# Optimization experiments

Hardware: AMD Instinct MI355X
Metric: run time of the kernel (lower is better)

## Reference

```python
import jax, jax.numpy as jnp
import numpy as np

N, D, H, DFF, NH = 8192, 128, 256, 2048, 2
HD = D // NH
DEG = 32
E = N * DEG
LN_EPS = 1e-5


def setup_inputs() -> dict:
    key = jax.random.key(0)
    ks = jax.random.split(key, 20)
    s = 0.02
    return {
        "x": jax.random.normal(ks[0], (N, D), jnp.float32),
        "edge_index": jax.random.randint(ks[1], (2, E), 0, N, jnp.int64),
        "beta": jnp.ones((), jnp.float32),  # AGNNConv learnable beta, init 1
        "in_proj_w": jax.random.normal(ks[2], (3 * D, D), jnp.float32) * s,
        "in_proj_b": jnp.zeros((3 * D,), jnp.float32),
        "out_proj_w": jax.random.normal(ks[3], (D, D), jnp.float32) * s,
        "out_proj_b": jnp.zeros((D,), jnp.float32),
        "ln1_g": jnp.ones((D,), jnp.float32),
        "ln1_b": jnp.zeros((D,), jnp.float32),
        "ff1_w": jax.random.normal(ks[4], (DFF, D), jnp.float32) * s,
        "ff1_b": jnp.zeros((DFF,), jnp.float32),
        "ff2_w": jax.random.normal(ks[5], (D, DFF), jnp.float32) * s,
        "ff2_b": jnp.zeros((D,), jnp.float32),
        "ln2_g": jnp.ones((D,), jnp.float32),
        "ln2_b": jnp.zeros((D,), jnp.float32),
        "fc_w": jax.random.normal(ks[6], (H, D), jnp.float32) * s,
        "fc_b": jnp.zeros((H,), jnp.float32),
        "head_w": jax.random.normal(ks[7], (2, H), jnp.float32) * s,
        "head_b": jnp.zeros((2,), jnp.float32),
    }


def _layernorm(x, g, b):
    mu = jnp.mean(x, axis=-1, keepdims=True)
    var = jnp.mean((x - mu) ** 2, axis=-1, keepdims=True)
    return (x - mu) * jax.lax.rsqrt(var + LN_EPS) * g + b


def _agnn(x, edge_index, beta):
    # PyG AGNNConv: add self-loops, cosine-sim attention, segment softmax over targets
    n = x.shape[0]
    loop = jnp.arange(n, dtype=edge_index.dtype)
    src = jnp.concatenate([edge_index[0], loop])  # message source j
    dst = jnp.concatenate([edge_index[1], loop])  # aggregation target i
    xn = x / jnp.maximum(jnp.linalg.norm(x, axis=-1, keepdims=True), 1e-12)
    alpha = beta * jnp.sum(xn[dst] * xn[src], axis=-1)  # [E+N]
    m = jax.ops.segment_max(alpha, dst, num_segments=n)
    e = jnp.exp(alpha - m[dst])
    z = jax.ops.segment_sum(e, dst, num_segments=n)
    w = e / z[dst]
    return jax.ops.segment_sum(w[:, None] * x[src], dst, num_segments=n)


def reference(x, edge_index, beta, in_proj_w, in_proj_b, out_proj_w, out_proj_b,
              ln1_g, ln1_b, ff1_w, ff1_b, ff2_w, ff2_b, ln2_g, ln2_b,
              fc_w, fc_b, head_w, head_b):
    h = _agnn(x, edge_index, beta)  # [N, D]
    # transformer sees shape [N, 1, D] with batch_first=False -> seq over all N nodes
    qkv = h @ in_proj_w.T + in_proj_b  # [N, 3D]
    q, k, v = jnp.split(qkv, 3, axis=-1)
    q = q.reshape(N, NH, HD).transpose(1, 0, 2)  # [h, N, hd]
    k = k.reshape(N, NH, HD).transpose(1, 0, 2)
    v = v.reshape(N, NH, HD).transpose(1, 0, 2)
    scores = jnp.einsum('hnd,hmd->hnm', q, k) / jnp.sqrt(jnp.float32(HD))
    attn = jax.nn.softmax(scores, axis=-1)
    o = jnp.einsum('hnm,hmd->hnd', attn, v).transpose(1, 0, 2).reshape(N, D)
    o = o @ out_proj_w.T + out_proj_b
    h = _layernorm(h + o, ln1_g, ln1_b)  # post-LN (norm_first=False)
    ff = jax.nn.relu(h @ ff1_w.T + ff1_b) @ ff2_w.T + ff2_b
    h = _layernorm(h + ff, ln2_g, ln2_b)
    h = jax.nn.relu(h @ fc_w.T + fc_b)
    return h @ head_w.T + head_b  # [N, 2]
```

## Files before the change

kernel.cpp:

```cpp
#include <hip/hip_runtime.h>


typedef __attribute__((ext_vector_type(4))) float  f32x4;
typedef __attribute__((ext_vector_type(8))) __bf16 bf16x8;

#define DEV __device__ __forceinline__

DEV unsigned short f2bf_bits(float f) {
  union { float f; unsigned u; } v; v.f = f;
  unsigned r = v.u + 0x7FFFu + ((v.u >> 16) & 1u);
  return (unsigned short)(r >> 16);
}

DEV __bf16 f2bf(float f) {
  union { unsigned short s; __bf16 b; } o; o.s = f2bf_bits(f);
  return o.b;
}

DEV f32x4 mfma16(bf16x8 a, bf16x8 b, f32x4 c) {
  return __builtin_amdgcn_mfma_f32_16x16x32_bf16(a, b, c, 0, 0, 0);
}

DEV bf16x8 ones8() {
  union { unsigned short s[8]; bf16x8 v; } u;
#pragma unroll
  for (int i = 0; i < 8; i++) u.s[i] = 0x3F80;
  return u.v;
}

DEV void ub8(bf16x8 v, float* f) {
  union { bf16x8 v; unsigned short s[8]; } u; u.v = v;
#pragma unroll
  for (int i = 0; i < 8; i++) {
    union { unsigned u; float f; } w; w.u = (unsigned)u.s[i] << 16;
    f[i] = w.f;
  }
}

#define GLD16(gp, lp) __builtin_amdgcn_global_load_lds(                        \
    (const __attribute__((address_space(1))) void*)(gp),                       \
    (__attribute__((address_space(3))) void*)(lp), 16, 0, 0)


__global__ __launch_bounds__(256) void k_prep(
    const float* __restrict__ x, float* __restrict__ inv,
    int* __restrict__ counts, const float* __restrict__ s0,
    const float* __restrict__ s1, const float* __restrict__ s2,
    const float* __restrict__ s3, const float* __restrict__ s4, __bf16* d0,
    __bf16* d1, __bf16* d2, __bf16* d3, __bf16* d4) {
  const int n0 = 384 * 128, n1 = 128 * 128, n2 = 2048 * 128, n3 = 128 * 2048,
            n4 = 256 * 128;
  if (blockIdx.x < 2048) {
    int lane = threadIdx.x & 63, w = threadIdx.x >> 6;
    int row = blockIdx.x * 4 + w;
    float2 v = ((const float2*)(x + (size_t)row * 128))[lane];
    float s = v.x * v.x + v.y * v.y;
#pragma unroll
    for (int m = 1; m < 64; m <<= 1) s += __shfl_xor(s, m);
    if (lane == 0) {
      inv[row] = 1.f / fmaxf(sqrtf(s), 1e-12f);
      counts[row] = 0;
    }
    return;
  }
  int t = (blockIdx.x - 2048) * 256 + threadIdx.x;
  if (t < n0) { d0[t] = f2bf(s0[t]); return; } t -= n0;
  if (t < n1) { d1[t] = f2bf(s1[t]); return; } t -= n1;
  if (t < n2) { d2[t] = f2bf(s2[t]); return; } t -= n2;
  if (t < n3) { d3[t] = f2bf(s3[t]); return; } t -= n3;
  if (t < n4) { d4[t] = f2bf(s4[t]); }
}


__global__ void k_count(const int* __restrict__ ei, int* __restrict__ counts,
                        int E) {
  int e = blockIdx.x * 256 + threadIdx.x;
  if (e < E) atomicAdd(&counts[ei[E + e]], 1);
}

__global__ __launch_bounds__(256) void k_scan(const int* __restrict__ counts,
                                              int* __restrict__ offs,
                                              int* __restrict__ cursor) {
  __shared__ int sums[256];
  int t = threadIdx.x, base = t * 32;
  int s = 0;
  for (int i = 0; i < 32; i++) s += counts[base + i];
  sums[t] = s;
  __syncthreads();
  for (int off = 1; off < 256; off <<= 1) {
    int v = (t >= off) ? sums[t - off] : 0;
    __syncthreads();
    sums[t] += v;
    __syncthreads();
  }
  int run = sums[t] - s;
  for (int i = 0; i < 32; i++) {
    offs[base + i] = run; cursor[base + i] = run;
    run += counts[base + i];
  }
  if (t == 255) offs[8192] = run;
}

__global__ void k_scatter(const int* __restrict__ ei, int* __restrict__ cursor,
                          int* __restrict__ csr, int E) {
  int e = blockIdx.x * 256 + threadIdx.x;
  if (e < E) {
    int dst = ei[E + e];
    int pos = atomicAdd(&cursor[dst], 1);
    csr[pos] = ei[e];
  }
}

__global__ __launch_bounds__(256) void k_agnn(
    const float* __restrict__ x, const int* __restrict__ csr,
    const int* __restrict__ offs, const float* __restrict__ inv,
    const float* __restrict__ betap, float* __restrict__ hf,
    __bf16* __restrict__ hb) {
  int lane = threadIdx.x & 63, w = threadIdx.x >> 6;
  int dst = blockIdx.x * 4 + w;
  float beta = *betap;
  float2 xd = ((const float2*)(x + (size_t)dst * 128))[lane];
  float invd = inv[dst];
  float sd = xd.x * xd.x + xd.y * xd.y;
#pragma unroll
  for (int m = 1; m < 64; m <<= 1) sd += __shfl_xor(sd, m);
  float z = __expf(beta * sd * invd * invd);
  float ax = z * xd.x, ay = z * xd.y;
  int e0 = offs[dst], e1 = offs[dst + 1];
  int e = e0;
  for (; e + 2 <= e1; e += 2) {
    int s0 = csr[e], s1 = csr[e + 1];
    float2 xa = ((const float2*)(x + (size_t)s0 * 128))[lane];
    float2 xb = ((const float2*)(x + (size_t)s1 * 128))[lane];
    float ia = inv[s0], ib = inv[s1];
    float da = xd.x * xa.x + xd.y * xa.y;
    float db = xd.x * xb.x + xd.y * xb.y;
#pragma unroll
    for (int m = 1; m < 64; m <<= 1) {
      da += __shfl_xor(da, m);
      db += __shfl_xor(db, m);
    }
    float sa = __expf(beta * da * invd * ia);
    float sb = __expf(beta * db * invd * ib);
    z += sa + sb;
    ax += sa * xa.x + sb * xb.x;
    ay += sa * xa.y + sb * xb.y;
  }
  if (e < e1) {
    int s0 = csr[e];
    float2 xa = ((const float2*)(x + (size_t)s0 * 128))[lane];
    float da = xd.x * xa.x + xd.y * xa.y;
#pragma unroll
    for (int m = 1; m < 64; m <<= 1) da += __shfl_xor(da, m);
    float sa = __expf(beta * da * invd * inv[s0]);
    z += sa; ax += sa * xa.x; ay += sa * xa.y;
  }
  float r = 1.f / z;
  ax *= r; ay *= r;
  float2 o; o.x = ax; o.y = ay;
  ((float2*)(hf + (size_t)dst * 128))[lane] = o;
  hb[(size_t)dst * 128 + 2 * lane]     = f2bf(ax);
  hb[(size_t)dst * 128 + 2 * lane + 1] = f2bf(ay);
}

__global__ __launch_bounds__(256, 2) void k_gemm(
    const __bf16* __restrict__ A, const __bf16* __restrict__ B,
    const float* __restrict__ bias, float* __restrict__ Cf,
    __bf16* __restrict__ Cb, float* __restrict__ Cpart, int M, int N, int K,
    int relu) {
  __shared__ __bf16 As[128 * 64];
  __shared__ __bf16 Bs[128 * 64];
  const int tid = threadIdx.x, lane = tid & 63, wid = tid >> 6;
  const int wm = wid & 1, wn = wid >> 1;
  const int bm = blockIdx.x * 128, bn = blockIdx.y * 128;
  const int kz = blockIdx.z, nkz = gridDim.z;
  const int kchunk = K / nkz, k0beg = kz * kchunk, k0end = k0beg + kchunk;
  const int lr = lane >> 3, lc8 = (lane & 7) * 8;
  const int l15 = lane & 15, quad = lane >> 4, kq = quad * 8;

  f32x4 acc[4][4] = {};
  const __bf16* Ab = A + (size_t)(bm + lr) * K + lc8;
  const __bf16* Bb = B + (size_t)(bn + lr) * K + lc8;

  for (int k0 = k0beg; k0 < k0end; k0 += 64) {
#pragma unroll
    for (int i = 0; i < 4; i++) {
      int j = wid * 4 + i;
      GLD16(Ab + (size_t)(8 * j) * K + k0, &As[j * 512]);
      GLD16(Bb + (size_t)(8 * j) * K + k0, &Bs[j * 512]);
    }
    __syncthreads();
    const int ar = (wm * 64 + l15) * 64 + kq;
    const int br = (wn * 64 + l15) * 64 + kq;
#pragma unroll
    for (int kk = 0; kk < 2; kk++) {
      bf16x8 a[4], b[4];
#pragma unroll
      for (int mt = 0; mt < 4; mt++)
        a[mt] = *(const bf16x8*)&As[ar + mt * 1024 + kk * 32];
#pragma unroll
      for (int nt = 0; nt < 4; nt++)
        b[nt] = *(const bf16x8*)&Bs[br + nt * 1024 + kk * 32];
#pragma unroll
      for (int mt = 0; mt < 4; mt++)
#pragma unroll
        for (int nt = 0; nt < 4; nt++)
          acc[mt][nt] = mfma16(a[mt], b[nt], acc[mt][nt]);
    }
    __syncthreads();
  }
  const int col0 = bn + wn * 64 + l15;
  const int row0 = bm + wm * 64 + quad * 4;
  if (Cpart) {
    float* P = Cpart + (size_t)kz * M * N;
#pragma unroll
    for (int mt = 0; mt < 4; mt++)
#pragma unroll
      for (int nt = 0; nt < 4; nt++)
#pragma unroll
        for (int r = 0; r < 4; r++)
          P[(size_t)(row0 + mt * 16 + r) * N + col0 + nt * 16] = acc[mt][nt][r];
  } else {
#pragma unroll
    for (int nt = 0; nt < 4; nt++) {
      float bv = bias[col0 + nt * 16];
#pragma unroll
      for (int mt = 0; mt < 4; mt++)
#pragma unroll
        for (int r = 0; r < 4; r++) {
          float v = acc[mt][nt][r] + bv;
          if (relu) v = fmaxf(v, 0.f);
          size_t idx = (size_t)(row0 + mt * 16 + r) * N + col0 + nt * 16;
          if (Cf) Cf[idx] = v;
          if (Cb) Cb[idx] = f2bf(v);
        }
    }
  }
}

__global__ __launch_bounds__(256, 2) void k_gemm_qkv(
    const __bf16* __restrict__ A, const __bf16* __restrict__ B,
    const float* __restrict__ bias, __bf16* __restrict__ Qb,
    __bf16* __restrict__ Kb, __bf16* __restrict__ Vtb) {
  __shared__ __bf16 smem[17408];
  __bf16* As = smem;
  __bf16* Bs = smem + 8192;
  const int K = 128;
  const int tid = threadIdx.x, lane = tid & 63, wid = tid >> 6;
  const int wm = wid & 1, wn = wid >> 1;
  const int bm = blockIdx.x * 128, y = blockIdx.y, bn = y * 128;
  const int lr = lane >> 3, lc8 = (lane & 7) * 8;
  const int l15 = lane & 15, quad = lane >> 4, kq = quad * 8;
  const float qscale = 0.125f * 1.44269504089f;

  f32x4 acc[4][4] = {};
  const __bf16* Ab = A + (size_t)(bm + lr) * K + lc8;
  const __bf16* Bb = B + (size_t)(bn + lr) * K + lc8;

  for (int k0 = 0; k0 < 128; k0 += 64) {
#pragma unroll
    for (int i = 0; i < 4; i++) {
      int j = wid * 4 + i;
      GLD16(Ab + (size_t)(8 * j) * K + k0, &As[j * 512]);
      GLD16(Bb + (size_t)(8 * j) * K + k0, &Bs[j * 512]);
    }
    __syncthreads();
    const int ar = (wm * 64 + l15) * 64 + kq;
    const int br = (wn * 64 + l15) * 64 + kq;
#pragma unroll
    for (int kk = 0; kk < 2; kk++) {
      bf16x8 a[4], b[4];
#pragma unroll
      for (int mt = 0; mt < 4; mt++)
        a[mt] = *(const bf16x8*)&As[ar + mt * 1024 + kk * 32];
#pragma unroll
      for (int nt = 0; nt < 4; nt++)
        b[nt] = *(const bf16x8*)&Bs[br + nt * 1024 + kk * 32];
#pragma unroll
      for (int mt = 0; mt < 4; mt++)
#pragma unroll
        for (int nt = 0; nt < 4; nt++)
          acc[mt][nt] = mfma16(a[mt], b[nt], acc[mt][nt]);
    }
    __syncthreads();
  }

  if (y < 2) {
    __bf16* D = (y == 0) ? Qb : Kb;
    float sc = (y == 0) ? qscale : 1.f;
    int h = wn;
#pragma unroll
    for (int nt = 0; nt < 4; nt++) {
      int c = wn * 64 + nt * 16 + l15;
      float bv = bias[bn + c];
      int d = nt * 16 + l15;
#pragma unroll
      for (int mt = 0; mt < 4; mt++)
#pragma unroll
        for (int r = 0; r < 4; r++) {
          int row = bm + wm * 64 + mt * 16 + quad * 4 + r;
          D[(size_t)h * 524288 + (size_t)row * 64 + d] =
              f2bf((acc[mt][nt][r] + bv) * sc);
        }
    }
  } else {
#pragma unroll
    for (int nt = 0; nt < 4; nt++) {
      int c = wn * 64 + nt * 16 + l15;
      float bv = bias[bn + c];
#pragma unroll
      for (int mt = 0; mt < 4; mt++)
#pragma unroll
        for (int r = 0; r < 4; r++) {
          int nl = wm * 64 + mt * 16 + quad * 4 + r;
          smem[nl * 136 + c] = f2bf(acc[mt][nt][r] + bv);
        }
    }
    __syncthreads();
    int d = tid >> 1, nh = tid & 1;
    __bf16* dst = Vtb + (size_t)d * 8192 + bm + nh * 64;
#pragma unroll
    for (int i = 0; i < 8; i++) {
      union { unsigned short s[8]; bf16x8 v; } u;
#pragma unroll
      for (int e = 0; e < 8; e++)
        u.s[e] = *(const unsigned short*)&smem[(nh * 64 + i * 8 + e) * 136 + d];
      *(bf16x8*)(dst + i * 8) = u.v;
    }
  }
}

__global__ __launch_bounds__(256, 4) void k_attn(
    const __bf16* __restrict__ Qb, const __bf16* __restrict__ Kb,
    const __bf16* __restrict__ Vtb, __bf16* __restrict__ Opart,
    float* __restrict__ Lpart) {
  __shared__ __bf16 Ks[4096];
  __shared__ __bf16 Vs[4096];
  __shared__ __bf16 Ps[4][32 * 88];

  const int tid = threadIdx.x, lane = tid & 63, w = tid >> 6;
  const int qt = blockIdx.x, h = blockIdx.y, kz = blockIdx.z;
  const int qbase = qt * 128;
  const int l15 = lane & 15, quad = lane >> 4;
  const int lofs = lane * 8;

  const __bf16* Qg = Qb + ((size_t)h * 8192 + qbase) * 64;
  const __bf16* Kg = Kb + (size_t)h * 8192 * 64;
  const __bf16* Vg = Vtb + (size_t)h * 64 * 8192;
  const bf16x8 vone = ones8();

#pragma unroll
  for (int i = 0; i < 2; i++) {
    int j = w * 2 + i;
    __bf16* dstb = (j < 4) ? &Ks[j * 1024] : &Vs[(j - 4) * 1024];
#pragma unroll
    for (int hh = 0; hh < 2; hh++)
      GLD16(Qg + (size_t)(j * 16 + l15) * 64 + hh * 32 + quad * 8,
            dstb + hh * 512);
  }
  __syncthreads();
  bf16x8 aq[2][2];
#pragma unroll
  for (int s = 0; s < 2; s++) {
    int j = w * 2 + s;
    const __bf16* base = (j < 4) ? &Ks[j * 1024] : &Vs[(j - 4) * 1024];
    aq[s][0] = *(const bf16x8*)&base[lofs];
    aq[s][1] = *(const bf16x8*)&base[512 + lofs];
  }
  __syncthreads();

  f32x4 o[2][4] = {};
  f32x4 lacc[2] = {};
  const int kstart = kz * 1024;

  for (int kt = 0; kt < 16; kt++) {
    int kb = kstart + kt * 64;
#pragma unroll
    for (int hh = 0; hh < 2; hh++) {
      GLD16(Kg + (size_t)(kb + w * 16 + l15) * 64 + hh * 32 + quad * 8,
            &Ks[w * 1024 + hh * 512]);
      GLD16(Vg + (size_t)(w * 16 + l15) * 8192 + kb + hh * 32 + quad * 8,
            &Vs[w * 1024 + hh * 512]);
    }
    __syncthreads();

#pragma unroll
    for (int mt = 0; mt < 4; mt++) {
      bf16x8 k0 = *(const bf16x8*)&Ks[mt * 1024 + lofs];
      bf16x8 k1 = *(const bf16x8*)&Ks[mt * 1024 + 512 + lofs];
#pragma unroll
      for (int s = 0; s < 2; s++) {
        f32x4 St = {};
        St = mfma16(k0, aq[s][0], St);
        St = mfma16(k1, aq[s][1], St);
        union { float f; unsigned u; } p0, p1, p2, p3;
        p0.f = __builtin_amdgcn_exp2f(St[0]);
        p1.f = __builtin_amdgcn_exp2f(St[1]);
        p2.f = __builtin_amdgcn_exp2f(St[2]);
        p3.f = __builtin_amdgcn_exp2f(St[3]);
        uint2 pk;
        pk.x = (p0.u >> 16) | (p1.u & 0xFFFF0000u);
        pk.y = (p2.u >> 16) | (p3.u & 0xFFFF0000u);
        *(uint2*)&Ps[w][(s * 16 + l15) * 88 + mt * 16 + quad * 4] = pk;
      }
    }
    bf16x8 vf[4][2];
#pragma unroll
    for (int nd = 0; nd < 4; nd++) {
      vf[nd][0] = *(const bf16x8*)&Vs[nd * 1024 + lofs];
      vf[nd][1] = *(const bf16x8*)&Vs[nd * 1024 + 512 + lofs];
    }
#pragma unroll
    for (int s = 0; s < 2; s++) {
      bf16x8 ap0 = *(const bf16x8*)&Ps[w][(s * 16 + l15) * 88 + quad * 8];
      bf16x8 ap1 = *(const bf16x8*)&Ps[w][(s * 16 + l15) * 88 + 32 + quad * 8];
      lacc[s] = mfma16(ap0, vone, lacc[s]);
      lacc[s] = mfma16(ap1, vone, lacc[s]);
#pragma unroll
      for (int nd = 0; nd < 4; nd++) {
        o[s][nd] = mfma16(ap0, vf[nd][0], o[s][nd]);
        o[s][nd] = mfma16(ap1, vf[nd][1], o[s][nd]);
      }
    }
    __syncthreads();
  }

  const size_t bpart = (size_t)(h * 8 + kz);
#pragma unroll
  for (int s = 0; s < 2; s++) {
#pragma unroll
    for (int nd = 0; nd < 4; nd++)
#pragma unroll
      for (int r = 0; r < 4; r++) {
        int row = qbase + w * 32 + s * 16 + quad * 4 + r;
        Opart[(bpart * 8192 + row) * 64 + nd * 16 + l15] = f2bf(o[s][nd][r]);
      }
    if (l15 == 0) {
#pragma unroll
      for (int r = 0; r < 4; r++) {
        int row = qbase + w * 32 + s * 16 + quad * 4 + r;
        Lpart[bpart * 8192 + row] = lacc[s][r];
      }
    }
  }
}

__global__ __launch_bounds__(256) void k_oproj_ln(
    const __bf16* __restrict__ Opart, const float* __restrict__ Lpart,
    const __bf16* __restrict__ Wo, const float* __restrict__ ob,
    const float* __restrict__ hf, const float* __restrict__ g,
    const float* __restrict__ bt, float* __restrict__ h1f,
    __bf16* __restrict__ h1b) {
  __shared__ __bf16 Af[4 * 2048];
  __shared__ __bf16 Bf[8 * 2048];
  __shared__ float scr1[64][2], scr2[64][2];
  const int tid = threadIdx.x, lane = tid & 63, w = tid >> 6;
  const int l15 = lane & 15, quad = lane >> 4;
  const int lofs = lane * 8;
  const int bm = blockIdx.x * 64;
  const int wm = w & 1, wn = w >> 1;

#pragma unroll
  for (int f = 0; f < 2; f++) {
    int j = w * 2 + f;
#pragma unroll
    for (int kq = 0; kq < 4; kq++)
      GLD16(Wo + (size_t)(j * 16 + l15) * 128 + kq * 32 + quad * 8,
            &Bf[j * 2048 + kq * 512]);
  }
  {
    int n = bm + w * 16 + l15;
    float L0 = 0.f, L1 = 0.f;
#pragma unroll
    for (int z = 0; z < 8; z++) {
      L0 += Lpart[(size_t)z * 8192 + n];
      L1 += Lpart[(size_t)(8 + z) * 8192 + n];
    }
    float r0 = 1.f / L0, r1 = 1.f / L1;
#pragma unroll
    for (int kq = 0; kq < 4; kq++) {
      int hh = kq >> 1;
      int d0 = (kq & 1) * 32 + quad * 8;
      float acc8[8] = {};
#pragma unroll
      for (int z = 0; z < 8; z++) {
        bf16x8 t = *(const bf16x8*)&Opart[((size_t)(hh * 8 + z) * 8192 + n) *
                                              64 + d0];
        float f[8];
        ub8(t, f);
#pragma unroll
        for (int e = 0; e < 8; e++) acc8[e] += f[e];
      }
      float rh = hh ? r1 : r0;
      union { unsigned short s[8]; bf16x8 v; } u;
#pragma unroll
      for (int e = 0; e < 8; e++) u.s[e] = f2bf_bits(acc8[e] * rh);
      *(bf16x8*)&Af[w * 2048 + kq * 512 + lane * 8] = u.v;
    }
  }
  __syncthreads();

  f32x4 acc[2][4] = {};
#pragma unroll
  for (int kq = 0; kq < 4; kq++) {
    bf16x8 a[2], b[4];
#pragma unroll
    for (int mt = 0; mt < 2; mt++)
      a[mt] = *(const bf16x8*)&Af[(wm * 2 + mt) * 2048 + kq * 512 + lofs];
#pragma unroll
    for (int nt = 0; nt < 4; nt++)
      b[nt] = *(const bf16x8*)&Bf[(wn * 4 + nt) * 2048 + kq * 512 + lofs];
#pragma unroll
    for (int mt = 0; mt < 2; mt++)
#pragma unroll
      for (int nt = 0; nt < 4; nt++)
        acc[mt][nt] = mfma16(a[mt], b[nt], acc[mt][nt]);
  }

  float v[2][4][4];
#pragma unroll
  for (int mt = 0; mt < 2; mt++)
#pragma unroll
    for (int r = 0; r < 4; r++) {
      int row = bm + wm * 32 + mt * 16 + quad * 4 + r;
      float s1 = 0.f, s2 = 0.f;
#pragma unroll
      for (int nt = 0; nt < 4; nt++) {
        int col = wn * 64 + nt * 16 + l15;
        float val = acc[mt][nt][r] + ob[col] + hf[(size_t)row * 128 + col];
        v[mt][nt][r] = val;
        s1 += val;
        s2 += val * val;
      }
#pragma unroll
      for (int msk = 1; msk < 16; msk <<= 1) {
        s1 += __shfl_xor(s1, msk);
        s2 += __shfl_xor(s2, msk);
      }
      if (l15 == 0) {
        int rl = wm * 32 + mt * 16 + quad * 4 + r;
        scr1[rl][wn] = s1;
        scr2[rl][wn] = s2;
      }
    }
  __syncthreads();
#pragma unroll
  for (int mt = 0; mt < 2; mt++)
#pragma unroll
    for (int r = 0; r < 4; r++) {
      int rl = wm * 32 + mt * 16 + quad * 4 + r;
      int row = bm + rl;
      float S1 = scr1[rl][0] + scr1[rl][1];
      float S2 = scr2[rl][0] + scr2[rl][1];
      float mu = S1 * (1.f / 128.f);
      float var = S2 * (1.f / 128.f) - mu * mu;
      float rstd = rsqrtf(var + 1e-5f);
#pragma unroll
      for (int nt = 0; nt < 4; nt++) {
        int col = wn * 64 + nt * 16 + l15;
        float y = (v[mt][nt][r] - mu) * rstd * g[col] + bt[col];
        h1f[(size_t)row * 128 + col] = y;
        h1b[(size_t)row * 128 + col] = f2bf(y);
      }
    }
}

__global__ __launch_bounds__(256) void k_addln4(
    const float* __restrict__ A, const float* __restrict__ part,
    const float* __restrict__ pbias, const float* __restrict__ g,
    const float* __restrict__ bt, __bf16* __restrict__ outb) {
  int lane = threadIdx.x & 63, w = threadIdx.x >> 6;
  int row = blockIdx.x * 4 + w;
  float2 a = ((const float2*)(A + (size_t)row * 128))[lane];
  float2 pb = ((const float2*)pbias)[lane];
  float sx = 0.f, sy = 0.f;
#pragma unroll
  for (int z = 0; z < 4; z++) {
    float2 p =
        ((const float2*)(part + (size_t)z * 1048576 + (size_t)row * 128))[lane];
    sx += p.x; sy += p.y;
  }
  float vx = a.x + pb.x + sx, vy = a.y + pb.y + sy;
  float s = vx + vy;
#pragma unroll
  for (int m = 1; m < 64; m <<= 1) s += __shfl_xor(s, m);
  float mu = s * (1.f / 128.f);
  float dx = vx - mu, dy = vy - mu;
  float q = dx * dx + dy * dy;
#pragma unroll
  for (int m = 1; m < 64; m <<= 1) q += __shfl_xor(q, m);
  float rstd = rsqrtf(q * (1.f / 128.f) + 1e-5f);
  float2 gg = ((const float2*)g)[lane];
  float2 bb = ((const float2*)bt)[lane];
  outb[(size_t)row * 128 + 2 * lane]     = f2bf(dx * rstd * gg.x + bb.x);
  outb[(size_t)row * 128 + 2 * lane + 1] = f2bf(dy * rstd * gg.y + bb.y);
}

__global__ __launch_bounds__(256) void k_fc_head(
    const __bf16* __restrict__ A, const __bf16* __restrict__ Wfc,
    const float* __restrict__ fcb, const float* __restrict__ hw,
    const float* __restrict__ hb, float* __restrict__ out) {
  __shared__ __bf16 Af[4 * 2048];
  __shared__ __bf16 Bf[16 * 2048];
  __shared__ float scr0[64][2], scr1[64][2];
  const int tid = threadIdx.x, lane = tid & 63, w = tid >> 6;
  const int l15 = lane & 15, quad = lane >> 4;
  const int lofs = lane * 8;
  const int bm = blockIdx.x * 64;
  const int wm = w & 1, wn = w >> 1;

#pragma unroll
  for (int kq = 0; kq < 4; kq++)
    GLD16(A + (size_t)(bm + w * 16 + l15) * 128 + kq * 32 + quad * 8,
          &Af[w * 2048 + kq * 512]);
#pragma unroll
  for (int f = 0; f < 4; f++) {
    int j = w * 4 + f;
#pragma unroll
    for (int kq = 0; kq < 4; kq++)
      GLD16(Wfc + (size_t)(j * 16 + l15) * 128 + kq * 32 + quad * 8,
            &Bf[j * 2048 + kq * 512]);
  }
  __syncthreads();

  f32x4 acc[2][8] = {};
#pragma unroll
  for (int kq = 0; kq < 4; kq++) {
    bf16x8 a[2], b[8];
#pragma unroll
    for (int mt = 0; mt < 2; mt++)
      a[mt] = *(const bf16x8*)&Af[(wm * 2 + mt) * 2048 + kq * 512 + lofs];
#pragma unroll
    for (int nt = 0; nt < 8; nt++)
      b[nt] = *(const bf16x8*)&Bf[(wn * 8 + nt) * 2048 + kq * 512 + lofs];
#pragma unroll
    for (int mt = 0; mt < 2; mt++)
#pragma unroll
      for (int nt = 0; nt < 8; nt++)
        acc[mt][nt] = mfma16(a[mt], b[nt], acc[mt][nt]);
  }

#pragma unroll
  for (int mt = 0; mt < 2; mt++)
#pragma unroll
    for (int r = 0; r < 4; r++) {
      float p0 = 0.f, p1 = 0.f;
#pragma unroll
      for (int nt = 0; nt < 8; nt++) {
        int col = wn * 128 + nt * 16 + l15;
        float vv = fmaxf(acc[mt][nt][r] + fcb[col], 0.f);
        p0 += vv * hw[col];
        p1 += vv * hw[256 + col];
      }
#pragma unroll
      for (int msk = 1; msk < 16; msk <<= 1) {
        p0 += __shfl_xor(p0, msk);
        p1 += __shfl_xor(p1, msk);
      }
      if (l15 == 0) {
        int rl = wm * 32 + mt * 16 + quad * 4 + r;
        scr0[rl][wn] = p0;
        scr1[rl][wn] = p1;
      }
    }
  __syncthreads();
  if (tid < 64) {
    out[(size_t)(bm + tid) * 2]     = scr0[tid][0] + scr0[tid][1] + hb[0];
    out[(size_t)(bm + tid) * 2 + 1] = scr1[tid][0] + scr1[tid][1] + hb[1];
  }
}

extern "C" void kernel_launch(void* const* d_in, const int* in_sizes, int n_in,
                              void* d_out, int out_size, void* d_ws,
                              size_t ws_size, hipStream_t stream) {
  const float* x     = (const float*)d_in[0];
  const int*   ei    = (const int*)d_in[1];
  const float* beta  = (const float*)d_in[2];
  const float* in_w  = (const float*)d_in[3];
  const float* in_b  = (const float*)d_in[4];
  const float* out_w = (const float*)d_in[5];
  const float* out_b = (const float*)d_in[6];
  const float* ln1g  = (const float*)d_in[7];
  const float* ln1b  = (const float*)d_in[8];
  const float* ff1w  = (const float*)d_in[9];
  const float* ff1b  = (const float*)d_in[10];
  const float* ff2w  = (const float*)d_in[11];
  const float* ff2b  = (const float*)d_in[12];
  const float* ln2g  = (const float*)d_in[13];
  const float* ln2b  = (const float*)d_in[14];
  const float* fcw   = (const float*)d_in[15];
  const float* fcb   = (const float*)d_in[16];
  const float* hw    = (const float*)d_in[17];
  const float* hbias = (const float*)d_in[18];
  float* out = (float*)d_out;
  const int N = 8192;
  const int E = in_sizes[1] / 2;

  char* wsp = (char*)d_ws;
  size_t off = 0;
  auto alloc = [&](size_t b) -> void* {
    void* p = wsp + off;
    off = (off + b + 255) & ~(size_t)255;
    return p;
  };

  float*  inv     = (float*)alloc((size_t)N * 4);
  int*    counts  = (int*)alloc((size_t)N * 4);
  int*    offs    = (int*)alloc((size_t)(N + 1) * 4);
  int*    cursor  = (int*)alloc((size_t)N * 4);
  int*    csr     = (int*)alloc((size_t)E * 4);
  float*  h_f     = (float*)alloc((size_t)N * 128 * 4);
  __bf16* h_b     = (__bf16*)alloc((size_t)N * 128 * 2);
  float*  h1_f    = (float*)alloc((size_t)N * 128 * 4);
  __bf16* h1_b    = (__bf16*)alloc((size_t)N * 128 * 2);
  __bf16* h2_b    = (__bf16*)alloc((size_t)N * 128 * 2);
  float*  Lpart   = (float*)alloc((size_t)16 * N * 4);
  __bf16* w_in    = (__bf16*)alloc((size_t)384 * 128 * 2);
  __bf16* w_out   = (__bf16*)alloc((size_t)128 * 128 * 2);
  __bf16* w_ff1   = (__bf16*)alloc((size_t)2048 * 128 * 2);
  __bf16* w_ff2   = (__bf16*)alloc((size_t)128 * 2048 * 2);
  __bf16* w_fc    = (__bf16*)alloc((size_t)256 * 128 * 2);
  char*   bigA    = (char*)alloc((size_t)16 * N * 64 * 4);
  __bf16* Opart   = (__bf16*)bigA;
  __bf16* ff1o    = (__bf16*)bigA;
  char*   bigB    = (char*)alloc((size_t)16777216);
  __bf16* Qb      = (__bf16*)bigB;
  __bf16* Kb      = (__bf16*)(bigB + 2097152);
  __bf16* Vtb     = (__bf16*)(bigB + 2 * 2097152);
  float*  ff2part = (float*)bigB;
  (void)ws_size; (void)n_in; (void)out_size;

  k_prep<<<4784, 256, 0, stream>>>(x, inv, counts, in_w, out_w, ff1w, ff2w,
                                   fcw, w_in, w_out, w_ff1, w_ff2, w_fc);
  k_count<<<(E + 255) / 256, 256, 0, stream>>>(ei, counts, E);
  k_scan<<<1, 256, 0, stream>>>(counts, offs, cursor);
  k_scatter<<<(E + 255) / 256, 256, 0, stream>>>(ei, cursor, csr, E);
  k_agnn<<<N / 4, 256, 0, stream>>>(x, csr, offs, inv, beta, h_f, h_b);

  k_gemm_qkv<<<dim3(64, 3), 256, 0, stream>>>(h_b, w_in, in_b, Qb, Kb, Vtb);
  k_attn<<<dim3(64, 2, 8), 256, 0, stream>>>(Qb, Kb, Vtb, Opart, Lpart);
  k_oproj_ln<<<128, 256, 0, stream>>>(Opart, Lpart, w_out, out_b, h_f, ln1g,
                                      ln1b, h1_f, h1_b);
  k_gemm<<<dim3(64, 16, 1), 256, 0, stream>>>(h1_b, w_ff1, ff1b, nullptr, ff1o,
                                              nullptr, N, 2048, 128, 1);
  k_gemm<<<dim3(64, 1, 4), 256, 0, stream>>>(ff1o, w_ff2, nullptr, nullptr,
                                             nullptr, ff2part, N, 128, 2048, 0);
  k_addln4<<<N / 4, 256, 0, stream>>>(h1_f, ff2part, ff2b, ln2g, ln2b, h2_b);
  k_fc_head<<<128, 256, 0, stream>>>(h2_b, w_fc, fcb, hw, hbias, out);
}
```

Measured before the change: 265.1 us.

## Double attention query tile per block and fuse add-LN2 into fc/head kernel

The attention kernel now gives each wave 64 query rows instead of 32 and uses half as many blocks. Q is staged through the enlarged P buffer, so each K/V tile loaded into shared memory is reused across twice as many queries. Separately, the residual add plus LayerNorm2 is fused into the fc/head kernel: two waves compute the normalized rows straight into shared memory while the other two load fc weights, which removes the h2 round trip and one launch. The cost is more registers and LDS per attention block (launch bound lowered to 2), fewer attention blocks, and fc_w reloaded by twice as many tail blocks.

After: 261.1 us. Within noise of the previous version (-1.5%).

```diff
diff --git a/kernel.cpp b/kernel.cpp
--- a/kernel.cpp
+++ b/kernel.cpp
@@ -330,17 +330,17 @@
   }
 }
 
-__global__ __launch_bounds__(256, 4) void k_attn(
+__global__ __launch_bounds__(256, 2) void k_attn(
     const __bf16* __restrict__ Qb, const __bf16* __restrict__ Kb,
     const __bf16* __restrict__ Vtb, __bf16* __restrict__ Opart,
     float* __restrict__ Lpart) {
   __shared__ __bf16 Ks[4096];
   __shared__ __bf16 Vs[4096];
-  __shared__ __bf16 Ps[4][32 * 88];
+  __shared__ __bf16 Ps[4][64 * 88];
 
   const int tid = threadIdx.x, lane = tid & 63, w = tid >> 6;
   const int qt = blockIdx.x, h = blockIdx.y, kz = blockIdx.z;
-  const int qbase = qt * 128;
+  const int qbase = qt * 256;
   const int l15 = lane & 15, quad = lane >> 4;
   const int lofs = lane * 8;
 
@@ -349,28 +349,27 @@
   const __bf16* Vg = Vtb + (size_t)h * 64 * 8192;
   const bf16x8 vone = ones8();
 
-#pragma unroll
-  for (int i = 0; i < 2; i++) {
-    int j = w * 2 + i;
-    __bf16* dstb = (j < 4) ? &Ks[j * 1024] : &Vs[(j - 4) * 1024];
+  __bf16* Qstage = &Ps[0][0];
+#pragma unroll
+  for (int i = 0; i < 4; i++) {
+    int j = w * 4 + i;
 #pragma unroll
     for (int hh = 0; hh < 2; hh++)
       GLD16(Qg + (size_t)(j * 16 + l15) * 64 + hh * 32 + quad * 8,
-            dstb + hh * 512);
+            Qstage + j * 1024 + hh * 512);
   }
   __syncthreads();
-  bf16x8 aq[2][2];
-#pragma unroll
-  for (int s = 0; s < 2; s++) {
-    int j = w * 2 + s;
-    const __bf16* base = (j < 4) ? &Ks[j * 1024] : &Vs[(j - 4) * 1024];
+  bf16x8 aq[4][2];
+#pragma unroll
+  for (int s = 0; s < 4; s++) {
+    const __bf16* base = Qstage + (size_t)(w * 4 + s) * 1024;
     aq[s][0] = *(const bf16x8*)&base[lofs];
     aq[s][1] = *(const bf16x8*)&base[512 + lofs];
   }
   __syncthreads();
 
-  f32x4 o[2][4] = {};
-  f32x4 lacc[2] = {};
+  f32x4 o[4][4] = {};
+  f32x4 lacc[4] = {};
   const int kstart = kz * 1024;
 
   for (int kt = 0; kt < 16; kt++) {
@@ -389,7 +388,7 @@
       bf16x8 k0 = *(const bf16x8*)&Ks[mt * 1024 + lofs];
       bf16x8 k1 = *(const bf16x8*)&Ks[mt * 1024 + 512 + lofs];
 #pragma unroll
-      for (int s = 0; s < 2; s++) {
+      for (int s = 0; s < 4; s++) {
         f32x4 St = {};
         St = mfma16(k0, aq[s][0], St);
         St = mfma16(k1, aq[s][1], St);
@@ -411,7 +410,7 @@
       vf[nd][1] = *(const bf16x8*)&Vs[nd * 1024 + 512 + lofs];
     }
 #pragma unroll
-    for (int s = 0; s < 2; s++) {
+    for (int s = 0; s < 4; s++) {
       bf16x8 ap0 = *(const bf16x8*)&Ps[w][(s * 16 + l15) * 88 + quad * 8];
       bf16x8 ap1 = *(const bf16x8*)&Ps[w][(s * 16 + l15) * 88 + 32 + quad * 8];
       lacc[s] = mfma16(ap0, vone, lacc[s]);
@@ -427,18 +426,18 @@
 
   const size_t bpart = (size_t)(h * 8 + kz);
 #pragma unroll
-  for (int s = 0; s < 2; s++) {
+  for (int s = 0; s < 4; s++) {
 #pragma unroll
     for (int nd = 0; nd < 4; nd++)
 #pragma unroll
       for (int r = 0; r < 4; r++) {
-        int row = qbase + w * 32 + s * 16 + quad * 4 + r;
+        int row = qbase + w * 64 + s * 16 + quad * 4 + r;
         Opart[(bpart * 8192 + row) * 64 + nd * 16 + l15] = f2bf(o[s][nd][r]);
       }
     if (l15 == 0) {
 #pragma unroll
       for (int r = 0; r < 4; r++) {
-        int row = qbase + w * 32 + s * 16 + quad * 4 + r;
+        int row = qbase + w * 64 + s * 16 + quad * 4 + r;
         Lpart[bpart * 8192 + row] = lacc[s][r];
       }
     }
@@ -565,78 +564,82 @@
     }
 }
 
-__global__ __launch_bounds__(256) void k_addln4(
-    const float* __restrict__ A, const float* __restrict__ part,
+__global__ __launch_bounds__(256) void k_tail(
+    const float* __restrict__ h1f, const float* __restrict__ part,
     const float* __restrict__ pbias, const float* __restrict__ g,
-    const float* __restrict__ bt, __bf16* __restrict__ outb) {
-  int lane = threadIdx.x & 63, w = threadIdx.x >> 6;
-  int row = blockIdx.x * 4 + w;
-  float2 a = ((const float2*)(A + (size_t)row * 128))[lane];
-  float2 pb = ((const float2*)pbias)[lane];
-  float sx = 0.f, sy = 0.f;
-#pragma unroll
-  for (int z = 0; z < 4; z++) {
-    float2 p =
-        ((const float2*)(part + (size_t)z * 1048576 + (size_t)row * 128))[lane];
-    sx += p.x; sy += p.y;
-  }
-  float vx = a.x + pb.x + sx, vy = a.y + pb.y + sy;
-  float s = vx + vy;
-#pragma unroll
-  for (int m = 1; m < 64; m <<= 1) s += __shfl_xor(s, m);
-  float mu = s * (1.f / 128.f);
-  float dx = vx - mu, dy = vy - mu;
-  float q = dx * dx + dy * dy;
-#pragma unroll
-  for (int m = 1; m < 64; m <<= 1) q += __shfl_xor(q, m);
-  float rstd = rsqrtf(q * (1.f / 128.f) + 1e-5f);
-  float2 gg = ((const float2*)g)[lane];
-  float2 bb = ((const float2*)bt)[lane];
-  outb[(size_t)row * 128 + 2 * lane]     = f2bf(dx * rstd * gg.x + bb.x);
-  outb[(size_t)row * 128 + 2 * lane + 1] = f2bf(dy * rstd * gg.y + bb.y);
-}
-
-__global__ __launch_bounds__(256) void k_fc_head(
-    const __bf16* __restrict__ A, const __bf16* __restrict__ Wfc,
+    const float* __restrict__ bt, const __bf16* __restrict__ Wfc,
     const float* __restrict__ fcb, const float* __restrict__ hw,
     const float* __restrict__ hb, float* __restrict__ out) {
-  __shared__ __bf16 Af[4 * 2048];
+  __shared__ __bf16 Af[2 * 2048];
   __shared__ __bf16 Bf[16 * 2048];
-  __shared__ float scr0[64][2], scr1[64][2];
+  __shared__ float scr0[32][4], scr1[32][4];
   const int tid = threadIdx.x, lane = tid & 63, w = tid >> 6;
   const int l15 = lane & 15, quad = lane >> 4;
   const int lofs = lane * 8;
-  const int bm = blockIdx.x * 64;
-  const int wm = w & 1, wn = w >> 1;
-
-#pragma unroll
-  for (int kq = 0; kq < 4; kq++)
-    GLD16(A + (size_t)(bm + w * 16 + l15) * 128 + kq * 32 + quad * 8,
-          &Af[w * 2048 + kq * 512]);
-#pragma unroll
-  for (int f = 0; f < 4; f++) {
-    int j = w * 4 + f;
-#pragma unroll
-    for (int kq = 0; kq < 4; kq++)
-      GLD16(Wfc + (size_t)(j * 16 + l15) * 128 + kq * 32 + quad * 8,
-            &Bf[j * 2048 + kq * 512]);
+  const int bm = blockIdx.x * 32;
+
+  if (w >= 2) {
+#pragma unroll
+    for (int f = 0; f < 8; f++) {
+      int j = (w - 2) * 8 + f;
+#pragma unroll
+      for (int kq = 0; kq < 4; kq++)
+        GLD16(Wfc + (size_t)(j * 16 + l15) * 128 + kq * 32 + quad * 8,
+              &Bf[j * 2048 + kq * 512]);
+    }
+  } else {
+    int row = bm + w * 16 + l15;
+    float val[4][8];
+    float s1 = 0.f, s2 = 0.f;
+#pragma unroll
+    for (int kq = 0; kq < 4; kq++) {
+      int c0 = kq * 32 + quad * 8;
+      const float* h1p = h1f + (size_t)row * 128 + c0;
+#pragma unroll
+      for (int j = 0; j < 8; j++) val[kq][j] = h1p[j] + pbias[c0 + j];
+#pragma unroll
+      for (int z = 0; z < 4; z++) {
+        const float* pp = part + (size_t)z * 1048576 + (size_t)row * 128 + c0;
+#pragma unroll
+        for (int j = 0; j < 8; j++) val[kq][j] += pp[j];
+      }
+#pragma unroll
+      for (int j = 0; j < 8; j++) {
+        s1 += val[kq][j];
+        s2 += val[kq][j] * val[kq][j];
+      }
+    }
+    s1 += __shfl_xor(s1, 16); s1 += __shfl_xor(s1, 32);
+    s2 += __shfl_xor(s2, 16); s2 += __shfl_xor(s2, 32);
+    float mu = s1 * (1.f / 128.f);
+    float var = s2 * (1.f / 128.f) - mu * mu;
+    float rstd = rsqrtf(var + 1e-5f);
+#pragma unroll
+    for (int kq = 0; kq < 4; kq++) {
+      int c0 = kq * 32 + quad * 8;
+      union { unsigned short s[8]; bf16x8 v; } u;
+#pragma unroll
+      for (int j = 0; j < 8; j++)
+        u.s[j] = f2bf_bits((val[kq][j] - mu) * rstd * g[c0 + j] + bt[c0 + j]);
+      *(bf16x8*)&Af[w * 2048 + kq * 512 + lane * 8] = u.v;
+    }
   }
   __syncthreads();
 
-  f32x4 acc[2][8] = {};
+  f32x4 acc[2][4] = {};
 #pragma unroll
   for (int kq = 0; kq < 4; kq++) {
-    bf16x8 a[2], b[8];
+    bf16x8 a[2], b[4];
 #pragma unroll
     for (int mt = 0; mt < 2; mt++)
-      a[mt] = *(const bf16x8*)&Af[(wm * 2 + mt) * 2048 + kq * 512 + lofs];
-#pragma unroll
-    for (int nt = 0; nt < 8; nt++)
-      b[nt] = *(const bf16x8*)&Bf[(wn * 8 + nt) * 2048 + kq * 512 + lofs];
+      a[mt] = *(const bf16x8*)&Af[mt * 2048 + kq * 512 + lofs];
+#pragma unroll
+    for (int nt = 0; nt < 4; nt++)
+      b[nt] = *(const bf16x8*)&Bf[(w * 4 + nt) * 2048 + kq * 512 + lofs];
 #pragma unroll
     for (int mt = 0; mt < 2; mt++)
 #pragma unroll
-      for (int nt = 0; nt < 8; nt++)
+      for (int nt = 0; nt < 4; nt++)
         acc[mt][nt] = mfma16(a[mt], b[nt], acc[mt][nt]);
   }
 
@@ -646,8 +649,8 @@
     for (int r = 0; r < 4; r++) {
       float p0 = 0.f, p1 = 0.f;
 #pragma unroll
-      for (int nt = 0; nt < 8; nt++) {
-        int col = wn * 128 + nt * 16 + l15;
+      for (int nt = 0; nt < 4; nt++) {
+        int col = w * 64 + nt * 16 + l15;
         float vv = fmaxf(acc[mt][nt][r] + fcb[col], 0.f);
         p0 += vv * hw[col];
         p1 += vv * hw[256 + col];
@@ -658,15 +661,17 @@
         p1 += __shfl_xor(p1, msk);
       }
       if (l15 == 0) {
-        int rl = wm * 32 + mt * 16 + quad * 4 + r;
-        scr0[rl][wn] = p0;
-        scr1[rl][wn] = p1;
+        int rl = mt * 16 + quad * 4 + r;
+        scr0[rl][w] = p0;
+        scr1[rl][w] = p1;
       }
     }
   __syncthreads();
-  if (tid < 64) {
-    out[(size_t)(bm + tid) * 2]     = scr0[tid][0] + scr0[tid][1] + hb[0];
-    out[(size_t)(bm + tid) * 2 + 1] = scr1[tid][0] + scr1[tid][1] + hb[1];
+  if (tid < 32) {
+    float p0 = scr0[tid][0] + scr0[tid][1] + scr0[tid][2] + scr0[tid][3];
+    float p1 = scr1[tid][0] + scr1[tid][1] + scr1[tid][2] + scr1[tid][3];
+    out[(size_t)(bm + tid) * 2]     = p0 + hb[0];
+    out[(size_t)(bm + tid) * 2 + 1] = p1 + hb[1];
   }
 }
 
@@ -713,7 +718,6 @@
   __bf16* h_b     = (__bf16*)alloc((size_t)N * 128 * 2);
   float*  h1_f    = (float*)alloc((size_t)N * 128 * 4);
   __bf16* h1_b    = (__bf16*)alloc((size_t)N * 128 * 2);
-  __bf16* h2_b    = (__bf16*)alloc((size_t)N * 128 * 2);
   float*  Lpart   = (float*)alloc((size_t)16 * N * 4);
   __bf16* w_in    = (__bf16*)alloc((size_t)384 * 128 * 2);
   __bf16* w_out   = (__bf16*)alloc((size_t)128 * 128 * 2);
@@ -738,13 +742,13 @@
   k_agnn<<<N / 4, 256, 0, stream>>>(x, csr, offs, inv, beta, h_f, h_b);
 
   k_gemm_qkv<<<dim3(64, 3), 256, 0, stream>>>(h_b, w_in, in_b, Qb, Kb, Vtb);
-  k_attn<<<dim3(64, 2, 8), 256, 0, stream>>>(Qb, Kb, Vtb, Opart, Lpart);
+  k_attn<<<dim3(32, 2, 8), 256, 0, stream>>>(Qb, Kb, Vtb, Opart, Lpart);
   k_oproj_ln<<<128, 256, 0, stream>>>(Opart, Lpart, w_out, out_b, h_f, ln1g,
                                       ln1b, h1_f, h1_b);
   k_gemm<<<dim3(64, 16, 1), 256, 0, stream>>>(h1_b, w_ff1, ff1b, nullptr, ff1o,
                                               nullptr, N, 2048, 128, 1);
   k_gemm<<<dim3(64, 1, 4), 256, 0, stream>>>(ff1o, w_ff2, nullptr, nullptr,
                                              nullptr, ff2part, N, 128, 2048, 0);
-  k_addln4<<<N / 4, 256, 0, stream>>>(h1_f, ff2part, ff2b, ln2g, ln2b, h2_b);
-  k_fc_head<<<128, 256, 0, stream>>>(h2_b, w_fc, fcb, hw, hbias, out);
-}
+  k_tail<<<256, 256, 0, stream>>>(h1_f, ff2part, ff2b, ln2g, ln2b, w_fc, fcb,
+                                  hw, hbias, out);
+}
```
